# Optimization experiments

Hardware: AMD Instinct MI355X
Metric: run time of the kernel (lower is better)

## Reference

```python
import jax, jax.numpy as jnp
import numpy as np

N_USERS = 10000
N_ITEMS = 40000
HID = 64
NNZ = 2_000_000
B = 8192
N_TOT = N_USERS + N_ITEMS
HOP = 3


def setup_inputs() -> dict:
    key = jax.random.key(0)
    ks = jax.random.split(key, 13)
    emb = lambda k, n: jax.random.normal(k, (n, HID), dtype=jnp.float32) * (1.0 / np.sqrt(HID))
    # Dense social adjacency; scaled so repeated propagation stays numerically stable
    S = jax.random.uniform(ks[6], (N_USERS, N_USERS), dtype=jnp.float32) * (2.0 / N_USERS)
    return {
        "users": jax.random.randint(ks[0], (B,), 0, N_USERS),
        "pos": jax.random.randint(ks[1], (B,), 0, N_ITEMS),
        "neg": jax.random.randint(ks[2], (B,), 0, N_ITEMS),
        "user_embs": emb(ks[3], N_USERS),
        "item_embs": emb(ks[4], N_ITEMS),
        "user1_embs": emb(ks[5], N_USERS),
        "item1_embs": emb(ks[7], N_ITEMS),
        "user2_embs": emb(ks[8], N_USERS),
        "item2_embs": emb(ks[9], N_ITEMS),
        "S": S,
        "A_rows": jax.random.randint(ks[10], (NNZ,), 0, N_TOT, dtype=jnp.int32),
        "A_cols": jax.random.randint(ks[11], (NNZ,), 0, N_TOT, dtype=jnp.int32),
        "A_vals": jax.random.uniform(ks[12], (NNZ,), dtype=jnp.float32) * (1.0 / 40.0),
        "hop": HOP,
    }


def social_gcn(uemb, S, hop):
    # LightGCN-style propagation over dense social graph; mean over layers 0..hop
    h = uemb
    acc = uemb
    for _ in range(hop):
        h = S @ h                      # [n_users, hid] dense GEMM
        acc = acc + h
    return acc / (hop + 1)


def ui_gcn(uemb, iemb, rows, cols, vals, hop):
    # LightGCN over sparse bipartite user-item graph of size [N_TOT, N_TOT]
    ego = jnp.concatenate([uemb, iemb], axis=0)   # [N_TOT, hid]
    h = ego
    acc = ego
    for _ in range(hop):
        msgs = vals[:, None] * h[cols]            # gather + scale  [nnz, hid]
        h = jax.ops.segment_sum(msgs, rows, num_segments=N_TOT)
        acc = acc + h
    out = acc / (hop + 1)
    return out[:N_USERS], out[N_USERS:]


def reference(users, pos, neg, user_embs, item_embs, user1_embs, item1_embs,
              user2_embs, item2_embs, S, A_rows, A_cols, A_vals, hop):
    all_user_S = social_gcn(user_embs, S, hop)
    all_user_A, all_item = ui_gcn(user_embs, item_embs, A_rows, A_cols, A_vals, hop)
    all_user = 0.5 * all_user_S + 0.5 * all_user_A

    all_user_social = social_gcn(user1_embs, S, hop)
    all_item_social = item1_embs
    all_user_rating, all_item_rating = ui_gcn(user2_embs, item2_embs, A_rows, A_cols, A_vals, hop)

    return (all_user[users], all_item[pos], all_item[neg],
            all_user_S, all_user_A,
            all_user_social[users], all_item_social[pos], all_item_social[neg],
            all_user_rating[users], all_item_rating[pos], all_item_rating[neg])
```

## Files before the change

kernel.cpp:

```cpp
#include <hip/hip_runtime.h>

#define N_USERS 10000
#define N_ITEMS 40000
#define N_TOTAL 50000
#define HID     64
#define BATCH   8192
#define HOPS    3
#define KDIM    10000
#define KTILES  157
#define KPAD    (KTILES * 64)
#define SPLITK  4

#define O0 0
#define O1 524288
#define O2 1048576
#define O3 1572864
#define O4 2212864
#define O5 2852864
#define O6 3377152
#define O7 3901440
#define O8 4425728
#define O9 4950016
#define O10 5474304

typedef __attribute__((ext_vector_type(8))) short short8;
typedef __attribute__((ext_vector_type(4))) float floatx4;
typedef __attribute__((ext_vector_type(4))) unsigned short ushort4v;
typedef __attribute__((ext_vector_type(8))) unsigned short ushort8v;

__device__ __forceinline__ unsigned short f32bf(float f) {
  union { float f; unsigned u; } v; v.f = f;
  unsigned r = v.u + 0x7fffu + ((v.u >> 16) & 1u);
  return (unsigned short)(r >> 16);
}

__global__ void init_social(const float* __restrict__ ue, const float* __restrict__ u1,
                            float* __restrict__ Hcur, float* __restrict__ Hacc) {
  int i = blockIdx.x * 256 + threadIdx.x;
  if (i >= N_USERS * HID) return;
  int r = i >> 6, c = i & 63;
  float a = ue[i], b = u1[i];
  size_t p = (size_t)r * 128 + c;
  Hcur[p] = a; Hcur[p + 64] = b;
  Hacc[p] = a; Hacc[p + 64] = b;
}

__global__ void init_ui(const float* __restrict__ ue, const float* __restrict__ ie,
                        const float* __restrict__ u2, const float* __restrict__ i2,
                        float* __restrict__ Ecur, float* __restrict__ Eacc) {
  int i = blockIdx.x * 256 + threadIdx.x;
  if (i >= N_TOTAL * HID) return;
  int r = i >> 6;
  float a, b;
  if (r < N_USERS) { a = ue[i]; b = u2[i]; }
  else             { a = ie[i - N_USERS * HID]; b = i2[i - N_USERS * HID]; }
  size_t p = (size_t)r * 128 + (i & 63);
  Ecur[p] = a; Ecur[p + 64] = b;
  Eacc[p] = a; Eacc[p + 64] = b;
}

__global__ void hist_rows(const int* __restrict__ rows, int* __restrict__ counts, int n) {
  int i = blockIdx.x * 256 + threadIdx.x;
  if (i < n) atomicAdd(&counts[rows[i]], 1);
}

__global__ void scan1(const int* __restrict__ counts, int* __restrict__ offs, int* __restrict__ bsum) {
  __shared__ int sh[256];
  int t = threadIdx.x;
  int base = blockIdx.x * 1024 + t * 4;
  int v0 = 0, v1 = 0, v2 = 0, v3 = 0;
  if (base + 0 < N_TOTAL) v0 = counts[base + 0];
  if (base + 1 < N_TOTAL) v1 = counts[base + 1];
  if (base + 2 < N_TOTAL) v2 = counts[base + 2];
  if (base + 3 < N_TOTAL) v3 = counts[base + 3];
  int s = v0 + v1 + v2 + v3;
  sh[t] = s;
  __syncthreads();
  for (int d = 1; d < 256; d <<= 1) {
    int x = (t >= d) ? sh[t - d] : 0;
    __syncthreads();
    sh[t] += x;
    __syncthreads();
  }
  int excl = sh[t] - s;
  if (t == 255) bsum[blockIdx.x] = sh[255];
  if (base + 0 < N_TOTAL) offs[base + 0] = excl; excl += v0;
  if (base + 1 < N_TOTAL) offs[base + 1] = excl; excl += v1;
  if (base + 2 < N_TOTAL) offs[base + 2] = excl; excl += v2;
  if (base + 3 < N_TOTAL) offs[base + 3] = excl;
}

__global__ void scan2(int* __restrict__ bsum, int nb) {
  __shared__ int sh[64];
  int t = threadIdx.x;
  int v = (t < nb) ? bsum[t] : 0;
  sh[t] = v;
  __syncthreads();
  for (int d = 1; d < 64; d <<= 1) {
    int x = (t >= d) ? sh[t - d] : 0;
    __syncthreads();
    sh[t] += x;
    __syncthreads();
  }
  if (t < nb) bsum[t] = sh[t] - v;
}

__global__ void scan3(int* __restrict__ offs, const int* __restrict__ bexcl,
                      int* __restrict__ cursor, int nnz) {
  int i = blockIdx.x * 256 + threadIdx.x;
  if (i < N_TOTAL) {
    int v = offs[i] + bexcl[i >> 10];
    offs[i] = v; cursor[i] = v;
  }
  if (i == 0) offs[N_TOTAL] = nnz;
}

__global__ void scatter_csr(const int* __restrict__ rows, const int* __restrict__ cols,
                            const float* __restrict__ vals, int* __restrict__ cursor,
                            int* __restrict__ ccol, float* __restrict__ cval, int n) {
  int i = blockIdx.x * 256 + threadIdx.x;
  if (i < n) {
    int p = atomicAdd(&cursor[rows[i]], 1);
    ccol[p] = cols[i];
    cval[p] = vals[i];
  }
}

__global__ __launch_bounds__(256)
void transpose_bf16(const float* __restrict__ H, unsigned short* __restrict__ Ht) {
  __shared__ __align__(16) float ts[64 * 132];
  int k0 = blockIdx.x * 64;
  int t = threadIdx.x;
#pragma unroll
  for (int i = 0; i < 8; i++) {
    int f = t + i * 256;
    int r = f >> 5, c4 = (f & 31) * 4;
    float4 v = make_float4(0.f, 0.f, 0.f, 0.f);
    if (k0 + r < KDIM) v = *(const float4*)&H[(size_t)(k0 + r) * 128 + c4];
    *(float4*)&ts[r * 132 + c4] = v;
  }
  __syncthreads();
#pragma unroll
  for (int i = 0; i < 4; i++) {
    int g = t + i * 256;
    int n = g >> 3, ko = (g & 7) * 8;
    ushort8v o;
#pragma unroll
    for (int j = 0; j < 8; j++) o[j] = f32bf(ts[(ko + j) * 132 + n]);
    *(ushort8v*)&Ht[(size_t)n * KPAD + k0 + ko] = o;
  }
}

__global__ __launch_bounds__(256)
void social_gemm(const float* __restrict__ S, const unsigned short* __restrict__ Bt,
                 float* __restrict__ C) {
  __shared__ __align__(16) unsigned short As[64 * 72];
  __shared__ __align__(16) unsigned short Bs[128 * 72];
  int m0 = blockIdx.x * 64;
  int ks = blockIdx.y;
  int t0 = (ks * KTILES) / SPLITK;
  int t1 = ((ks + 1) * KTILES) / SPLITK;
  int tid = threadIdx.x;
  int wave = tid >> 6, lane = tid & 63;
  int mq = lane & 15, quad = lane >> 4;

  floatx4 acc[8];
#pragma unroll
  for (int i = 0; i < 8; i++) acc[i] = (floatx4){0.f, 0.f, 0.f, 0.f};

  int ar = tid >> 2;
  int aq = tid & 3;
  bool rok = (m0 + ar) < KDIM;
  const float* arow = S + (size_t)(m0 + ar) * KDIM;
  int bn = tid >> 3;
  int bk = (tid & 7) * 8;

  for (int t = t0; t < t1; ++t) {
    int k0 = t * 64;
#pragma unroll
    for (int i = 0; i < 4; i++) {
      int kk = k0 + aq * 16 + i * 4;
      float4 v = make_float4(0.f, 0.f, 0.f, 0.f);
      if (rok && kk < KDIM) v = *(const float4*)(arow + kk);
      ushort4v b4;
      b4.x = f32bf(v.x); b4.y = f32bf(v.y); b4.z = f32bf(v.z); b4.w = f32bf(v.w);
      *(ushort4v*)&As[ar * 72 + aq * 16 + i * 4] = b4;
    }
#pragma unroll
    for (int i = 0; i < 4; i++) {
      int n = bn + i * 32;
      *(ushort8v*)&Bs[n * 72 + bk] = *(const ushort8v*)&Bt[(size_t)n * KPAD + k0 + bk];
    }
    __syncthreads();
#pragma unroll
    for (int kk = 0; kk < 64; kk += 32) {
      short8 a = *(const short8*)&As[(wave * 16 + mq) * 72 + kk + quad * 8];
#pragma unroll
      for (int nt = 0; nt < 8; nt++) {
        short8 b = *(const short8*)&Bs[(nt * 16 + mq) * 72 + kk + quad * 8];
        acc[nt] = __builtin_amdgcn_mfma_f32_16x16x32_bf16(a, b, acc[nt], 0, 0, 0);
      }
    }
    __syncthreads();
  }
#pragma unroll
  for (int nt = 0; nt < 8; nt++) {
    int col = nt * 16 + mq;
    int rbase = m0 + wave * 16 + quad * 4;
#pragma unroll
    for (int i = 0; i < 4; i++) {
      int r = rbase + i;
      if (r < KDIM) atomicAdd(&C[(size_t)r * 128 + col], acc[nt][i]);
    }
  }
}

__global__ __launch_bounds__(256)
void ui_hop(const int* __restrict__ offs, const int* __restrict__ ccol,
            const float* __restrict__ cval, const float* __restrict__ Ein,
            float* __restrict__ Eout) {
  int wid = blockIdx.x * 4 + (threadIdx.x >> 6);
  int lane = threadIdx.x & 63;
  int s = offs[wid], e = offs[wid + 1];
  float ax = 0.f, ay = 0.f;
  int j = s;
  for (; j + 4 <= e; j += 4) {
    int c0 = ccol[j], c1 = ccol[j + 1], c2 = ccol[j + 2], c3 = ccol[j + 3];
    float w0 = cval[j], w1 = cval[j + 1], w2 = cval[j + 2], w3 = cval[j + 3];
    float2 p0 = *(const float2*)&Ein[(size_t)c0 * 128 + lane * 2];
    float2 p1 = *(const float2*)&Ein[(size_t)c1 * 128 + lane * 2];
    float2 p2 = *(const float2*)&Ein[(size_t)c2 * 128 + lane * 2];
    float2 p3 = *(const float2*)&Ein[(size_t)c3 * 128 + lane * 2];
    ax += w0 * p0.x + w1 * p1.x + w2 * p2.x + w3 * p3.x;
    ay += w0 * p0.y + w1 * p1.y + w2 * p2.y + w3 * p3.y;
  }
  for (; j < e; ++j) {
    int c = ccol[j]; float w = cval[j];
    float2 p = *(const float2*)&Ein[(size_t)c * 128 + lane * 2];
    ax += w * p.x; ay += w * p.y;
  }
  float2 o; o.x = ax; o.y = ay;
  *(float2*)&Eout[(size_t)wid * 128 + lane * 2] = o;
}

__global__ void acc_add(float* __restrict__ acc, const float* __restrict__ h, int n4) {
  int i = blockIdx.x * 256 + threadIdx.x;
  if (i < n4) {
    float4* a = (float4*)acc;
    const float4* b = (const float4*)h;
    float4 x = a[i], y = b[i];
    x.x += y.x; x.y += y.y; x.z += y.z; x.w += y.w;
    a[i] = x;
  }
}

__global__ void full_out(const float* __restrict__ HSacc, const float* __restrict__ Eacc,
                         float* __restrict__ out) {
  int i = blockIdx.x * 256 + threadIdx.x;
  if (i >= N_USERS * HID) return;
  int r = i >> 6, c = i & 63;
  out[O3 + i] = HSacc[(size_t)r * 128 + c] * 0.25f;
  out[O4 + i] = Eacc[(size_t)r * 128 + c] * 0.25f;
}

__global__ void gather_out(const int* __restrict__ users, const int* __restrict__ pos,
                           const int* __restrict__ neg, const float* __restrict__ HSacc,
                           const float* __restrict__ Eacc, const float* __restrict__ item1,
                           float* __restrict__ out) {
  int b = blockIdx.x * 4 + (threadIdx.x >> 6);
  int lane = threadIdx.x & 63;
  int u = users[b], p = pos[b], n = neg[b];
  const float q = 0.25f;
  float us = HSacc[(size_t)u * 128 + lane] * q;
  float ua = Eacc[(size_t)u * 128 + lane] * q;
  size_t bl = (size_t)b * 64 + lane;
  out[O0 + bl]  = 0.5f * (us + ua);
  out[O1 + bl]  = Eacc[(size_t)(N_USERS + p) * 128 + lane] * q;
  out[O2 + bl]  = Eacc[(size_t)(N_USERS + n) * 128 + lane] * q;
  out[O5 + bl]  = HSacc[(size_t)u * 128 + 64 + lane] * q;
  out[O6 + bl]  = item1[(size_t)p * 64 + lane];
  out[O7 + bl]  = item1[(size_t)n * 64 + lane];
  out[O8 + bl]  = Eacc[(size_t)u * 128 + 64 + lane] * q;
  out[O9 + bl]  = Eacc[(size_t)(N_USERS + p) * 128 + 64 + lane] * q;
  out[O10 + bl] = Eacc[(size_t)(N_USERS + n) * 128 + 64 + lane] * q;
}

extern "C" void kernel_launch(void* const* d_in, const int* in_sizes, int n_in,
                              void* d_out, int out_size, void* d_ws, size_t ws_size,
                              hipStream_t stream) {
  (void)n_in; (void)out_size; (void)ws_size;
  const int*   users = (const int*)d_in[0];
  const int*   pos   = (const int*)d_in[1];
  const int*   neg   = (const int*)d_in[2];
  const float* ue    = (const float*)d_in[3];
  const float* ie    = (const float*)d_in[4];
  const float* u1    = (const float*)d_in[5];
  const float* i1    = (const float*)d_in[6];
  const float* u2    = (const float*)d_in[7];
  const float* i2    = (const float*)d_in[8];
  const float* S     = (const float*)d_in[9];
  const int*   Arows = (const int*)d_in[10];
  const int*   Acols = (const int*)d_in[11];
  const float* Avals = (const float*)d_in[12];
  const int nnz = in_sizes[10];

  char* ws = (char*)d_ws;
  size_t off = 0;
  auto alloc = [&](size_t b) { size_t r = off; off += (b + 255) & ~(size_t)255; return r; };
  float* HS0   = (float*)(ws + alloc(sizeof(float) * (size_t)N_USERS * 128));
  float* HS1   = (float*)(ws + alloc(sizeof(float) * (size_t)N_USERS * 128));
  float* HSacc = (float*)(ws + alloc(sizeof(float) * (size_t)N_USERS * 128));
  unsigned short* Ht = (unsigned short*)(ws + alloc(sizeof(short) * (size_t)128 * KPAD));
  float* E0    = (float*)(ws + alloc(sizeof(float) * (size_t)N_TOTAL * 128));
  float* E1    = (float*)(ws + alloc(sizeof(float) * (size_t)N_TOTAL * 128));
  float* Eacc  = (float*)(ws + alloc(sizeof(float) * (size_t)N_TOTAL * 128));
  int* counts  = (int*)(ws + alloc(sizeof(int) * (N_TOTAL + 16)));
  int* offs    = (int*)(ws + alloc(sizeof(int) * (N_TOTAL + 16)));
  int* cursor  = (int*)(ws + alloc(sizeof(int) * (N_TOTAL + 16)));
  int* bsum    = (int*)(ws + alloc(sizeof(int) * 256));
  int* ccol    = (int*)(ws + alloc(sizeof(int) * (size_t)nnz));
  float* cval  = (float*)(ws + alloc(sizeof(float) * (size_t)nnz));

  init_social<<<2500, 256, 0, stream>>>(ue, u1, HS0, HSacc);
  init_ui<<<12500, 256, 0, stream>>>(ue, ie, u2, i2, E0, Eacc);

  hipMemsetAsync(counts, 0, sizeof(int) * (N_TOTAL + 16), stream);
  hist_rows<<<(nnz + 255) / 256, 256, 0, stream>>>(Arows, counts, nnz);
  scan1<<<49, 256, 0, stream>>>(counts, offs, bsum);
  scan2<<<1, 64, 0, stream>>>(bsum, 49);
  scan3<<<196, 256, 0, stream>>>(offs, bsum, cursor, nnz);
  scatter_csr<<<(nnz + 255) / 256, 256, 0, stream>>>(Arows, Acols, Avals, cursor, ccol, cval, nnz);

  float* hc = HS0; float* hn = HS1;
  float* ec = E0;  float* en = E1;
  for (int h = 0; h < HOPS; ++h) {
    transpose_bf16<<<KTILES, 256, 0, stream>>>(hc, Ht);
    hipMemsetAsync(hn, 0, sizeof(float) * (size_t)N_USERS * 128, stream);
    social_gemm<<<dim3(KTILES, SPLITK), 256, 0, stream>>>(S, Ht, hn);
    acc_add<<<1250, 256, 0, stream>>>(HSacc, hn, (N_USERS * 128) / 4);
    { float* t = hc; hc = hn; hn = t; }
    ui_hop<<<12500, 256, 0, stream>>>(offs, ccol, cval, ec, en);
    acc_add<<<6250, 256, 0, stream>>>(Eacc, en, (N_TOTAL * 128) / 4);
    { float* t = ec; ec = en; en = t; }
  }

  float* out = (float*)d_out;
  full_out<<<2500, 256, 0, stream>>>(HSacc, Eacc, out);
  gather_out<<<2048, 256, 0, stream>>>(users, pos, neg, HSacc, Eacc, i1, out);
}
```

Before: 1.629 ms.

## Fuse social GEMM and sparse hop per layer, cache bf16 S, merge launches

Runs the dense social GEMM and the sparse user-item hop as branches of one launch per hop, so the two independent workloads share the GPU concurrently. The first hop converts S to bf16 and stores it in a workspace buffer, and later hops read that half-size copy instead of re-converting the fp32 matrix. The edge column and value arrays are packed into int2 pairs. Accumulator adds, memsets, init, histogram, scan, transpose and output kernels are merged to cut launch count and extra passes. This adds a large bf16 workspace buffer and more complex block-index dispatch, and the GEMM branch and sparse branch now compete for the same CUs.

Measured after the change: 1.895 ms. +16.3%, slower.

```diff
diff --git a/kernel.cpp b/kernel.cpp
--- a/kernel.cpp
+++ b/kernel.cpp
@@ -10,6 +10,7 @@
 #define KTILES  157
 #define KPAD    (KTILES * 64)
 #define SPLITK  4
+#define NSOC    (KTILES * SPLITK)
 
 #define O0 0
 #define O1 524288
@@ -34,34 +35,35 @@
   return (unsigned short)(r >> 16);
 }
 
-__global__ void init_social(const float* __restrict__ ue, const float* __restrict__ u1,
-                            float* __restrict__ Hcur, float* __restrict__ Hacc) {
-  int i = blockIdx.x * 256 + threadIdx.x;
-  if (i >= N_USERS * HID) return;
-  int r = i >> 6, c = i & 63;
-  float a = ue[i], b = u1[i];
-  size_t p = (size_t)r * 128 + c;
-  Hcur[p] = a; Hcur[p + 64] = b;
-  Hacc[p] = a; Hacc[p + 64] = b;
-}
-
-__global__ void init_ui(const float* __restrict__ ue, const float* __restrict__ ie,
-                        const float* __restrict__ u2, const float* __restrict__ i2,
-                        float* __restrict__ Ecur, float* __restrict__ Eacc) {
-  int i = blockIdx.x * 256 + threadIdx.x;
-  if (i >= N_TOTAL * HID) return;
-  int r = i >> 6;
-  float a, b;
-  if (r < N_USERS) { a = ue[i]; b = u2[i]; }
-  else             { a = ie[i - N_USERS * HID]; b = i2[i - N_USERS * HID]; }
-  size_t p = (size_t)r * 128 + (i & 63);
-  Ecur[p] = a; Ecur[p + 64] = b;
-  Eacc[p] = a; Eacc[p + 64] = b;
-}
-
-__global__ void hist_rows(const int* __restrict__ rows, int* __restrict__ counts, int n) {
-  int i = blockIdx.x * 256 + threadIdx.x;
-  if (i < n) atomicAdd(&counts[rows[i]], 1);
+__global__ __launch_bounds__(256)
+void init_all(const float* __restrict__ ue, const float* __restrict__ u1,
+              const float* __restrict__ ie, const float* __restrict__ u2,
+              const float* __restrict__ i2, const int* __restrict__ Arows,
+              int* __restrict__ counts, int nnz,
+              float* __restrict__ HS0, float* __restrict__ HS1, float* __restrict__ HSacc,
+              float* __restrict__ E0, float* __restrict__ Eacc) {
+  int b = blockIdx.x, t = threadIdx.x;
+  if (b < 2500) {
+    int i = b * 256 + t;
+    int r = i >> 6, c = i & 63;
+    float a = ue[i], x = u1[i];
+    size_t p = (size_t)r * 128 + c;
+    HS0[p] = a; HS0[p + 64] = x;
+    HSacc[p] = a; HSacc[p + 64] = x;
+    HS1[p] = 0.f; HS1[p + 64] = 0.f;
+  } else if (b < 15000) {
+    int i = (b - 2500) * 256 + t;
+    int r = i >> 6;
+    float a, x;
+    if (r < N_USERS) { a = ue[i]; x = u2[i]; }
+    else             { a = ie[i - N_USERS * HID]; x = i2[i - N_USERS * HID]; }
+    size_t p = (size_t)r * 128 + (i & 63);
+    E0[p] = a; E0[p + 64] = x;
+    Eacc[p] = a; Eacc[p + 64] = x;
+  } else {
+    int i = (b - 15000) * 256 + t;
+    if (i < nnz) atomicAdd(&counts[Arows[i]], 1);
+  }
 }
 
 __global__ void scan1(const int* __restrict__ counts, int* __restrict__ offs, int* __restrict__ bsum) {
@@ -105,31 +107,10 @@
   if (t < nb) bsum[t] = sh[t] - v;
 }
 
-__global__ void scan3(int* __restrict__ offs, const int* __restrict__ bexcl,
-                      int* __restrict__ cursor, int nnz) {
-  int i = blockIdx.x * 256 + threadIdx.x;
-  if (i < N_TOTAL) {
-    int v = offs[i] + bexcl[i >> 10];
-    offs[i] = v; cursor[i] = v;
-  }
-  if (i == 0) offs[N_TOTAL] = nnz;
-}
-
-__global__ void scatter_csr(const int* __restrict__ rows, const int* __restrict__ cols,
-                            const float* __restrict__ vals, int* __restrict__ cursor,
-                            int* __restrict__ ccol, float* __restrict__ cval, int n) {
-  int i = blockIdx.x * 256 + threadIdx.x;
-  if (i < n) {
-    int p = atomicAdd(&cursor[rows[i]], 1);
-    ccol[p] = cols[i];
-    cval[p] = vals[i];
-  }
-}
-
-__global__ __launch_bounds__(256)
-void transpose_bf16(const float* __restrict__ H, unsigned short* __restrict__ Ht) {
-  __shared__ __align__(16) float ts[64 * 132];
-  int k0 = blockIdx.x * 64;
+__device__ __forceinline__ void transpose_dev(int kb, const float* __restrict__ H,
+                                              unsigned short* __restrict__ Ht,
+                                              float* __restrict__ ts) {
+  int k0 = kb * 64;
   int t = threadIdx.x;
 #pragma unroll
   for (int i = 0; i < 8; i++) {
@@ -152,137 +133,192 @@
 }
 
 __global__ __launch_bounds__(256)
-void social_gemm(const float* __restrict__ S, const unsigned short* __restrict__ Bt,
-                 float* __restrict__ C) {
+void scan3_tr(int* __restrict__ offs, const int* __restrict__ bexcl,
+              int* __restrict__ cursor, int nnz,
+              const float* __restrict__ hc, unsigned short* __restrict__ Ht) {
+  __shared__ __align__(16) float ts[64 * 132];
+  if (blockIdx.x < 196) {
+    int i = blockIdx.x * 256 + threadIdx.x;
+    if (i < N_TOTAL) {
+      int v = offs[i] + bexcl[i >> 10];
+      offs[i] = v; cursor[i] = v;
+    }
+    if (i == 0) offs[N_TOTAL] = nnz;
+  } else {
+    transpose_dev(blockIdx.x - 196, hc, Ht, ts);
+  }
+}
+
+__global__ void scatter_csr(const int* __restrict__ rows, const int* __restrict__ cols,
+                            const float* __restrict__ vals, int* __restrict__ cursor,
+                            int2* __restrict__ edges, int n) {
+  int i = blockIdx.x * 256 + threadIdx.x;
+  if (i < n) {
+    int p = atomicAdd(&cursor[rows[i]], 1);
+    edges[p] = make_int2(cols[i], __float_as_int(vals[i]));
+  }
+}
+
+template<int H>
+__global__ __launch_bounds__(256)
+void hop_kernel(const float* __restrict__ S, unsigned short* __restrict__ Sb,
+                const unsigned short* __restrict__ Bt, float* __restrict__ Cdst,
+                const int* __restrict__ offs, const int2* __restrict__ edges,
+                const float* __restrict__ Ein, float* __restrict__ Eout,
+                float* __restrict__ Eacc) {
   __shared__ __align__(16) unsigned short As[64 * 72];
   __shared__ __align__(16) unsigned short Bs[128 * 72];
-  int m0 = blockIdx.x * 64;
-  int ks = blockIdx.y;
-  int t0 = (ks * KTILES) / SPLITK;
-  int t1 = ((ks + 1) * KTILES) / SPLITK;
   int tid = threadIdx.x;
-  int wave = tid >> 6, lane = tid & 63;
-  int mq = lane & 15, quad = lane >> 4;
-
-  floatx4 acc[8];
-#pragma unroll
-  for (int i = 0; i < 8; i++) acc[i] = (floatx4){0.f, 0.f, 0.f, 0.f};
-
-  int ar = tid >> 2;
-  int aq = tid & 3;
-  bool rok = (m0 + ar) < KDIM;
-  const float* arow = S + (size_t)(m0 + ar) * KDIM;
-  int bn = tid >> 3;
-  int bk = (tid & 7) * 8;
-
-  for (int t = t0; t < t1; ++t) {
-    int k0 = t * 64;
-#pragma unroll
-    for (int i = 0; i < 4; i++) {
-      int kk = k0 + aq * 16 + i * 4;
-      float4 v = make_float4(0.f, 0.f, 0.f, 0.f);
-      if (rok && kk < KDIM) v = *(const float4*)(arow + kk);
-      ushort4v b4;
-      b4.x = f32bf(v.x); b4.y = f32bf(v.y); b4.z = f32bf(v.z); b4.w = f32bf(v.w);
-      *(ushort4v*)&As[ar * 72 + aq * 16 + i * 4] = b4;
-    }
-#pragma unroll
-    for (int i = 0; i < 4; i++) {
-      int n = bn + i * 32;
-      *(ushort8v*)&Bs[n * 72 + bk] = *(const ushort8v*)&Bt[(size_t)n * KPAD + k0 + bk];
-    }
-    __syncthreads();
-#pragma unroll
-    for (int kk = 0; kk < 64; kk += 32) {
-      short8 a = *(const short8*)&As[(wave * 16 + mq) * 72 + kk + quad * 8];
-#pragma unroll
-      for (int nt = 0; nt < 8; nt++) {
-        short8 b = *(const short8*)&Bs[(nt * 16 + mq) * 72 + kk + quad * 8];
-        acc[nt] = __builtin_amdgcn_mfma_f32_16x16x32_bf16(a, b, acc[nt], 0, 0, 0);
+  if (blockIdx.x < NSOC) {
+    int mt = blockIdx.x % KTILES;
+    int ks = blockIdx.x / KTILES;
+    int m0 = mt * 64;
+    int t0 = (ks * KTILES) / SPLITK;
+    int t1 = ((ks + 1) * KTILES) / SPLITK;
+    int wave = tid >> 6, lane = tid & 63;
+    int mq = lane & 15, quad = lane >> 4;
+
+    floatx4 acc[8];
+#pragma unroll
+    for (int i = 0; i < 8; i++) acc[i] = (floatx4){0.f, 0.f, 0.f, 0.f};
+
+    int ar = tid >> 2;
+    int aq = tid & 3;
+    bool rok = (m0 + ar) < KDIM;
+    const float* arow = S + (size_t)(m0 + ar) * KDIM;
+    unsigned short* sbrow = Sb + (size_t)(m0 + ar) * KPAD;
+    int bn = tid >> 3;
+    int bk = (tid & 7) * 8;
+
+    for (int t = t0; t < t1; ++t) {
+      int k0 = t * 64;
+      if (H == 0) {
+#pragma unroll
+        for (int i = 0; i < 4; i++) {
+          int kk = k0 + aq * 16 + i * 4;
+          floatx4 v = (floatx4){0.f, 0.f, 0.f, 0.f};
+          if (rok && kk < KDIM) v = __builtin_nontemporal_load((const floatx4*)(arow + kk));
+          ushort4v b4;
+          b4[0] = f32bf(v[0]); b4[1] = f32bf(v[1]); b4[2] = f32bf(v[2]); b4[3] = f32bf(v[3]);
+          *(ushort4v*)&As[ar * 72 + aq * 16 + i * 4] = b4;
+          if (rok) __builtin_nontemporal_store(b4, (ushort4v*)&sbrow[kk]);
+        }
+      } else {
+        int koff = aq * 16;
+        ushort8v x0 = {0,0,0,0,0,0,0,0}, x1 = {0,0,0,0,0,0,0,0};
+        if (rok) {
+          x0 = __builtin_nontemporal_load((const ushort8v*)&sbrow[k0 + koff]);
+          x1 = __builtin_nontemporal_load((const ushort8v*)&sbrow[k0 + koff + 8]);
+        }
+        *(ushort8v*)&As[ar * 72 + koff] = x0;
+        *(ushort8v*)&As[ar * 72 + koff + 8] = x1;
       }
-    }
-    __syncthreads();
-  }
-#pragma unroll
-  for (int nt = 0; nt < 8; nt++) {
-    int col = nt * 16 + mq;
-    int rbase = m0 + wave * 16 + quad * 4;
-#pragma unroll
-    for (int i = 0; i < 4; i++) {
-      int r = rbase + i;
-      if (r < KDIM) atomicAdd(&C[(size_t)r * 128 + col], acc[nt][i]);
-    }
-  }
-}
-
-__global__ __launch_bounds__(256)
-void ui_hop(const int* __restrict__ offs, const int* __restrict__ ccol,
-            const float* __restrict__ cval, const float* __restrict__ Ein,
-            float* __restrict__ Eout) {
-  int wid = blockIdx.x * 4 + (threadIdx.x >> 6);
-  int lane = threadIdx.x & 63;
-  int s = offs[wid], e = offs[wid + 1];
-  float ax = 0.f, ay = 0.f;
-  int j = s;
-  for (; j + 4 <= e; j += 4) {
-    int c0 = ccol[j], c1 = ccol[j + 1], c2 = ccol[j + 2], c3 = ccol[j + 3];
-    float w0 = cval[j], w1 = cval[j + 1], w2 = cval[j + 2], w3 = cval[j + 3];
-    float2 p0 = *(const float2*)&Ein[(size_t)c0 * 128 + lane * 2];
-    float2 p1 = *(const float2*)&Ein[(size_t)c1 * 128 + lane * 2];
-    float2 p2 = *(const float2*)&Ein[(size_t)c2 * 128 + lane * 2];
-    float2 p3 = *(const float2*)&Ein[(size_t)c3 * 128 + lane * 2];
-    ax += w0 * p0.x + w1 * p1.x + w2 * p2.x + w3 * p3.x;
-    ay += w0 * p0.y + w1 * p1.y + w2 * p2.y + w3 * p3.y;
-  }
-  for (; j < e; ++j) {
-    int c = ccol[j]; float w = cval[j];
-    float2 p = *(const float2*)&Ein[(size_t)c * 128 + lane * 2];
-    ax += w * p.x; ay += w * p.y;
-  }
-  float2 o; o.x = ax; o.y = ay;
-  *(float2*)&Eout[(size_t)wid * 128 + lane * 2] = o;
-}
-
-__global__ void acc_add(float* __restrict__ acc, const float* __restrict__ h, int n4) {
-  int i = blockIdx.x * 256 + threadIdx.x;
-  if (i < n4) {
-    float4* a = (float4*)acc;
-    const float4* b = (const float4*)h;
-    float4 x = a[i], y = b[i];
-    x.x += y.x; x.y += y.y; x.z += y.z; x.w += y.w;
-    a[i] = x;
-  }
-}
-
-__global__ void full_out(const float* __restrict__ HSacc, const float* __restrict__ Eacc,
-                         float* __restrict__ out) {
-  int i = blockIdx.x * 256 + threadIdx.x;
-  if (i >= N_USERS * HID) return;
-  int r = i >> 6, c = i & 63;
-  out[O3 + i] = HSacc[(size_t)r * 128 + c] * 0.25f;
-  out[O4 + i] = Eacc[(size_t)r * 128 + c] * 0.25f;
-}
-
-__global__ void gather_out(const int* __restrict__ users, const int* __restrict__ pos,
-                           const int* __restrict__ neg, const float* __restrict__ HSacc,
-                           const float* __restrict__ Eacc, const float* __restrict__ item1,
-                           float* __restrict__ out) {
-  int b = blockIdx.x * 4 + (threadIdx.x >> 6);
-  int lane = threadIdx.x & 63;
-  int u = users[b], p = pos[b], n = neg[b];
-  const float q = 0.25f;
-  float us = HSacc[(size_t)u * 128 + lane] * q;
-  float ua = Eacc[(size_t)u * 128 + lane] * q;
-  size_t bl = (size_t)b * 64 + lane;
-  out[O0 + bl]  = 0.5f * (us + ua);
-  out[O1 + bl]  = Eacc[(size_t)(N_USERS + p) * 128 + lane] * q;
-  out[O2 + bl]  = Eacc[(size_t)(N_USERS + n) * 128 + lane] * q;
-  out[O5 + bl]  = HSacc[(size_t)u * 128 + 64 + lane] * q;
-  out[O6 + bl]  = item1[(size_t)p * 64 + lane];
-  out[O7 + bl]  = item1[(size_t)n * 64 + lane];
-  out[O8 + bl]  = Eacc[(size_t)u * 128 + 64 + lane] * q;
-  out[O9 + bl]  = Eacc[(size_t)(N_USERS + p) * 128 + 64 + lane] * q;
-  out[O10 + bl] = Eacc[(size_t)(N_USERS + n) * 128 + 64 + lane] * q;
+#pragma unroll
+      for (int i = 0; i < 4; i++) {
+        int n = bn + i * 32;
+        *(ushort8v*)&Bs[n * 72 + bk] = *(const ushort8v*)&Bt[(size_t)n * KPAD + k0 + bk];
+      }
+      __syncthreads();
+#pragma unroll
+      for (int kk = 0; kk < 64; kk += 32) {
+        short8 a = *(const short8*)&As[(wave * 16 + mq) * 72 + kk + quad * 8];
+#pragma unroll
+        for (int nt = 0; nt < 8; nt++) {
+          short8 b = *(const short8*)&Bs[(nt * 16 + mq) * 72 + kk + quad * 8];
+          acc[nt] = __builtin_amdgcn_mfma_f32_16x16x32_bf16(a, b, acc[nt], 0, 0, 0);
+        }
+      }
+      __syncthreads();
+    }
+#pragma unroll
+    for (int nt = 0; nt < 8; nt++) {
+      int col = nt * 16 + mq;
+      int rbase = m0 + wave * 16 + quad * 4;
+#pragma unroll
+      for (int i = 0; i < 4; i++) {
+        int r = rbase + i;
+        if (r < KDIM) atomicAdd(&Cdst[(size_t)r * 128 + col], acc[nt][i]);
+      }
+    }
+  } else {
+    int wid = (blockIdx.x - NSOC) * 4 + (tid >> 6);
+    int lane2 = (tid & 63) * 2;
+    const float* Einl = Ein + lane2;
+    int s = offs[wid], e = offs[wid + 1];
+    float ax = 0.f, ay = 0.f;
+    int j = s;
+    for (; j + 4 <= e; j += 4) {
+      int2 e0 = edges[j], e1 = edges[j + 1], e2 = edges[j + 2], e3 = edges[j + 3];
+      float2 p0 = *(const float2*)&Einl[(size_t)e0.x * 128];
+      float2 p1 = *(const float2*)&Einl[(size_t)e1.x * 128];
+      float2 p2 = *(const float2*)&Einl[(size_t)e2.x * 128];
+      float2 p3 = *(const float2*)&Einl[(size_t)e3.x * 128];
+      float w0 = __int_as_float(e0.y), w1 = __int_as_float(e1.y);
+      float w2 = __int_as_float(e2.y), w3 = __int_as_float(e3.y);
+      ax += w0 * p0.x + w1 * p1.x + w2 * p2.x + w3 * p3.x;
+      ay += w0 * p0.y + w1 * p1.y + w2 * p2.y + w3 * p3.y;
+    }
+    for (; j < e; ++j) {
+      int2 ed = edges[j];
+      float2 p = *(const float2*)&Einl[(size_t)ed.x * 128];
+      float w = __int_as_float(ed.y);
+      ax += w * p.x; ay += w * p.y;
+    }
+    size_t op = (size_t)wid * 128 + lane2;
+    if (H < 2) { float2 o; o.x = ax; o.y = ay; *(float2*)&Eout[op] = o; }
+    float2 a = *(float2*)&Eacc[op];
+    a.x += ax; a.y += ay;
+    *(float2*)&Eacc[op] = a;
+  }
+}
+
+template<int H>
+__global__ __launch_bounds__(256)
+void prep_kernel(const float* __restrict__ hc, unsigned short* __restrict__ Ht,
+                 float* __restrict__ HSacc, float* __restrict__ hn) {
+  __shared__ __align__(16) float ts[64 * 132];
+  if (blockIdx.x < KTILES) {
+    transpose_dev(blockIdx.x, hc, Ht, ts);
+  } else {
+    int i = (blockIdx.x - KTILES) * 256 + threadIdx.x;
+    if (i < (N_USERS * 128) / 4) {
+      float4 h = ((const float4*)hc)[i];
+      float4 a = ((float4*)HSacc)[i];
+      a.x += h.x; a.y += h.y; a.z += h.z; a.w += h.w;
+      ((float4*)HSacc)[i] = a;
+      if (H == 1) ((float4*)hn)[i] = make_float4(0.f, 0.f, 0.f, 0.f);
+    }
+  }
+}
+
+__global__ __launch_bounds__(256)
+void out_kernel(const int* __restrict__ users, const int* __restrict__ pos,
+                const int* __restrict__ neg, const float* __restrict__ HSacc,
+                const float* __restrict__ Eacc, const float* __restrict__ item1,
+                float* __restrict__ out) {
+  if (blockIdx.x < 2500) {
+    int i = blockIdx.x * 256 + threadIdx.x;
+    int r = i >> 6, c = i & 63;
+    out[O3 + i] = HSacc[(size_t)r * 128 + c] * 0.25f;
+    out[O4 + i] = Eacc[(size_t)r * 128 + c] * 0.25f;
+  } else {
+    int b = (blockIdx.x - 2500) * 4 + (threadIdx.x >> 6);
+    int lane = threadIdx.x & 63;
+    int u = users[b], p = pos[b], n = neg[b];
+    const float q = 0.25f;
+    float us = HSacc[(size_t)u * 128 + lane] * q;
+    float ua = Eacc[(size_t)u * 128 + lane] * q;
+    size_t bl = (size_t)b * 64 + lane;
+    out[O0 + bl]  = 0.5f * (us + ua);
+    out[O1 + bl]  = Eacc[(size_t)(N_USERS + p) * 128 + lane] * q;
+    out[O2 + bl]  = Eacc[(size_t)(N_USERS + n) * 128 + lane] * q;
+    out[O5 + bl]  = HSacc[(size_t)u * 128 + 64 + lane] * q;
+    out[O6 + bl]  = item1[(size_t)p * 64 + lane];
+    out[O7 + bl]  = item1[(size_t)n * 64 + lane];
+    out[O8 + bl]  = Eacc[(size_t)u * 128 + 64 + lane] * q;
+    out[O9 + bl]  = Eacc[(size_t)(N_USERS + p) * 128 + 64 + lane] * q;
+    out[O10 + bl] = Eacc[(size_t)(N_USERS + n) * 128 + 64 + lane] * q;
+  }
 }
 
 extern "C" void kernel_launch(void* const* d_in, const int* in_sizes, int n_in,
@@ -311,6 +347,7 @@
   float* HS1   = (float*)(ws + alloc(sizeof(float) * (size_t)N_USERS * 128));
   float* HSacc = (float*)(ws + alloc(sizeof(float) * (size_t)N_USERS * 128));
   unsigned short* Ht = (unsigned short*)(ws + alloc(sizeof(short) * (size_t)128 * KPAD));
+  unsigned short* Sb = (unsigned short*)(ws + alloc(sizeof(short) * (size_t)KDIM * KPAD));
   float* E0    = (float*)(ws + alloc(sizeof(float) * (size_t)N_TOTAL * 128));
   float* E1    = (float*)(ws + alloc(sizeof(float) * (size_t)N_TOTAL * 128));
   float* Eacc  = (float*)(ws + alloc(sizeof(float) * (size_t)N_TOTAL * 128));
@@ -318,33 +355,24 @@
   int* offs    = (int*)(ws + alloc(sizeof(int) * (N_TOTAL + 16)));
   int* cursor  = (int*)(ws + alloc(sizeof(int) * (N_TOTAL + 16)));
   int* bsum    = (int*)(ws + alloc(sizeof(int) * 256));
-  int* ccol    = (int*)(ws + alloc(sizeof(int) * (size_t)nnz));
-  float* cval  = (float*)(ws + alloc(sizeof(float) * (size_t)nnz));
-
-  init_social<<<2500, 256, 0, stream>>>(ue, u1, HS0, HSacc);
-  init_ui<<<12500, 256, 0, stream>>>(ue, ie, u2, i2, E0, Eacc);
+  int2* edges  = (int2*)(ws + alloc(sizeof(int2) * (size_t)nnz));
+
+  const int histB = (nnz + 255) / 256;
 
   hipMemsetAsync(counts, 0, sizeof(int) * (N_TOTAL + 16), stream);
-  hist_rows<<<(nnz + 255) / 256, 256, 0, stream>>>(Arows, counts, nnz);
+  init_all<<<15000 + histB, 256, 0, stream>>>(ue, u1, ie, u2, i2, Arows, counts, nnz,
+                                              HS0, HS1, HSacc, E0, Eacc);
   scan1<<<49, 256, 0, stream>>>(counts, offs, bsum);
   scan2<<<1, 64, 0, stream>>>(bsum, 49);
-  scan3<<<196, 256, 0, stream>>>(offs, bsum, cursor, nnz);
-  scatter_csr<<<(nnz + 255) / 256, 256, 0, stream>>>(Arows, Acols, Avals, cursor, ccol, cval, nnz);
-
-  float* hc = HS0; float* hn = HS1;
-  float* ec = E0;  float* en = E1;
-  for (int h = 0; h < HOPS; ++h) {
-    transpose_bf16<<<KTILES, 256, 0, stream>>>(hc, Ht);
-    hipMemsetAsync(hn, 0, sizeof(float) * (size_t)N_USERS * 128, stream);
-    social_gemm<<<dim3(KTILES, SPLITK), 256, 0, stream>>>(S, Ht, hn);
-    acc_add<<<1250, 256, 0, stream>>>(HSacc, hn, (N_USERS * 128) / 4);
-    { float* t = hc; hc = hn; hn = t; }
-    ui_hop<<<12500, 256, 0, stream>>>(offs, ccol, cval, ec, en);
-    acc_add<<<6250, 256, 0, stream>>>(Eacc, en, (N_TOTAL * 128) / 4);
-    { float* t = ec; ec = en; en = t; }
-  }
+  scan3_tr<<<196 + KTILES, 256, 0, stream>>>(offs, bsum, cursor, nnz, HS0, Ht);
+  scatter_csr<<<histB, 256, 0, stream>>>(Arows, Acols, Avals, cursor, edges, nnz);
+
+  hop_kernel<0><<<NSOC + 12500, 256, 0, stream>>>(S, Sb, Ht, HS1, offs, edges, E0, E1, Eacc);
+  prep_kernel<1><<<KTILES + 1250, 256, 0, stream>>>(HS1, Ht, HSacc, HS0);
+  hop_kernel<1><<<NSOC + 12500, 256, 0, stream>>>(S, Sb, Ht, HS0, offs, edges, E1, E0, Eacc);
+  prep_kernel<2><<<KTILES + 1250, 256, 0, stream>>>(HS0, Ht, HSacc, HS1);
+  hop_kernel<2><<<NSOC + 12500, 256, 0, stream>>>(S, Sb, Ht, HSacc, offs, edges, E0, E1, Eacc);
 
   float* out = (float*)d_out;
-  full_out<<<2500, 256, 0, stream>>>(HSacc, Eacc, out);
-  gather_out<<<2048, 256, 0, stream>>>(users, pos, neg, HSacc, Eacc, i1, out);
-}
+  out_kernel<<<2500 + 2048, 256, 0, stream>>>(users, pos, neg, HSacc, Eacc, i1, out);
+}
```
